# Performance work log

Hardware: AMD Instinct MI355X
Metric: run time of the kernel (lower is better)

The kernel has to match this reference:

```python
import jax, jax.numpy as jnp
import numpy as np

N_NODES = 100000
N_EDGES = 1600000


def setup_inputs() -> dict:
    key = jax.random.key(0)
    ks = jax.random.split(key, 12)
    s = lambda d: 1.0 / np.sqrt(d)
    inp = {
        "x": jax.random.normal(ks[0], (N_NODES, 64), dtype=jnp.float32),
        "edge_index": jax.random.randint(ks[1], (2, N_EDGES), 0, N_NODES, dtype=jnp.int64),
        "W_embed": jax.random.normal(ks[2], (64, 128), dtype=jnp.float32) * s(64),
        "eps1": jnp.zeros((), jnp.float32),
        "w1a": jax.random.normal(ks[3], (128, 128), dtype=jnp.float32) * s(128),
        "b1a": jnp.zeros((128,), jnp.float32),
        "w1b": jax.random.normal(ks[4], (128, 128), dtype=jnp.float32) * s(128),
        "b1b": jnp.zeros((128,), jnp.float32),
        "eps2": jnp.zeros((), jnp.float32),
        "w2a": jax.random.normal(ks[5], (128, 256), dtype=jnp.float32) * s(128),
        "b2a": jnp.zeros((256,), jnp.float32),
        "w2b": jax.random.normal(ks[6], (256, 128), dtype=jnp.float32) * s(256),
        "b2b": jnp.zeros((128,), jnp.float32),
        "eps3": jnp.zeros((), jnp.float32),
        "w3a": jax.random.normal(ks[7], (128, 256), dtype=jnp.float32) * s(128),
        "b3a": jnp.zeros((256,), jnp.float32),
        "w3b": jax.random.normal(ks[8], (256, 128), dtype=jnp.float32) * s(256),
        "b3b": jnp.zeros((128,), jnp.float32),
    }
    return inp


def _aggregate(h, src, dst, n):
    # GINConv sum aggregation: out[i] = sum_{(j,i) in E} h[j]
    return jax.ops.segment_sum(h[src], dst, num_segments=n)


def reference(x, edge_index, W_embed, eps1, w1a, b1a, w1b, b1b,
              eps2, w2a, b2a, w2b, b2b, eps3, w3a, b3a, w3b, b3b):
    src, dst = edge_index[0], edge_index[1]
    n = x.shape[0]
    # node_attr_encoder: linear embedding (dropout p=0 -> identity)
    h = x @ W_embed  # [N, dim]
    # conv1: nn((1+eps)*h + sum_neighbors), nn = Lin->ReLU->Lin
    z = (1.0 + eps1) * h + _aggregate(h, src, dst, n)
    h = jax.nn.relu(z @ w1a + b1a) @ w1b + b1b
    # conv2/conv3: nn = Lin->ReLU->Lin->ReLU
    z = (1.0 + eps2) * h + _aggregate(h, src, dst, n)
    h = jax.nn.relu(jax.nn.relu(z @ w2a + b2a) @ w2b + b2b)
    z = (1.0 + eps3) * h + _aggregate(h, src, dst, n)
    h = jax.nn.relu(jax.nn.relu(z @ w3a + b3a) @ w3b + b3b)
    return h
```

## Files before the change

kernel.cpp:

```cpp
#include <hip/hip_runtime.h>
#include <hip/hip_bf16.h>
#include <stdint.h>


typedef __attribute__((ext_vector_type(8))) short short8;
typedef __attribute__((ext_vector_type(16))) float float16v;

#define BKT 512
#define NBMAX 256

__device__ __forceinline__ float b2f_lo(unsigned int u) {
    return __uint_as_float(u << 16);
}
__device__ __forceinline__ float b2f_hi(unsigned int u) {
    return __uint_as_float(u & 0xffff0000u);
}
__device__ __forceinline__ unsigned short f2b(float f) {
    unsigned int u = __float_as_uint(f);
    return (unsigned short)((u + 0x7fffu + ((u >> 16) & 1u)) >> 16);
}

__global__ void detect_i64_kernel(const unsigned int* ei, int* flag) {
    if (threadIdx.x == 0) {
        int is64 = 1;
        for (int e = 0; e < 64; ++e)
            if (ei[2 * e + 1] != 0u) { is64 = 0; break; }
        *flag = is64;
    }
}

__device__ __forceinline__ int edge_at(const int* ei32, int is64, long long pos) {
    if (is64) return (int)(((const long long*)ei32)[pos]);
    return ei32[pos];
}

__global__ __launch_bounds__(256) void part_hist_kernel(
        const int* __restrict__ ei, const int* __restrict__ flag,
        int* __restrict__ bh, int E, int NB, int PB) {
    __shared__ int h[NBMAX];
    const int g = blockIdx.x, tid = threadIdx.x;
    const int is64 = *flag;
    for (int i = tid; i < NB; i += 256) h[i] = 0;
    __syncthreads();
    const int e0 = g * PB, e1 = min(e0 + PB, E);
    for (int e = e0 + tid; e < e1; e += 256) {
        int d = edge_at(ei, is64, (long long)E + e);
        atomicAdd(&h[d >> 9], 1);
    }
    __syncthreads();
    for (int i = tid; i < NB; i += 256) bh[i * gridDim.x + g] = h[i];
}

__global__ __launch_bounds__(1024) void scan1_kernel(
        const int* __restrict__ in, int* __restrict__ out,
        int* __restrict__ partial, int n) {
    __shared__ int sm[1024];
    const int t = threadIdx.x;
    const int i = blockIdx.x * 1024 + t;
    int v = (i < n) ? in[i] : 0;
    sm[t] = v;
    __syncthreads();
#pragma unroll
    for (int off = 1; off < 1024; off <<= 1) {
        int x = (t >= off) ? sm[t - off] : 0;
        __syncthreads();
        sm[t] += x;
        __syncthreads();
    }
    if (i < n) out[i] = sm[t] - v;
    if (t == 1023) partial[blockIdx.x] = sm[1023];
}

__global__ __launch_bounds__(256) void scan2_kernel(
        int* __restrict__ partial, int* __restrict__ blockoff, int g1) {
    __shared__ int sm[256];
    const int t = threadIdx.x;
    int v = (t < g1) ? partial[t] : 0;
    sm[t] = v;
    __syncthreads();
#pragma unroll
    for (int off = 1; off < 256; off <<= 1) {
        int x = (t >= off) ? sm[t - off] : 0;
        __syncthreads();
        sm[t] += x;
        __syncthreads();
    }
    blockoff[t] = sm[t] - v;
}

__global__ __launch_bounds__(1024) void scan3g_kernel(
        int* __restrict__ a, const int* __restrict__ blockoff, int n) {
    int i = blockIdx.x * 1024 + threadIdx.x;
    if (i < n) a[i] += blockoff[blockIdx.x];
}

__global__ __launch_bounds__(256) void part_scatter_kernel(
        const int* __restrict__ ei, const int* __restrict__ flag,
        const int* __restrict__ bhs, unsigned int* __restrict__ staged,
        int E, int NB, int PB) {
    __shared__ int cur[NBMAX];
    const int g = blockIdx.x, tid = threadIdx.x;
    const int is64 = *flag;
    for (int i = tid; i < NB; i += 256) cur[i] = bhs[i * gridDim.x + g];
    __syncthreads();
    const int e0 = g * PB, e1 = min(e0 + PB, E);
    for (int e = e0 + tid; e < e1; e += 256) {
        int d = edge_at(ei, is64, (long long)E + e);
        int s = edge_at(ei, is64, (long long)e);
        int b = d >> 9;
        int p = atomicAdd(&cur[b], 1);
        staged[p] = ((unsigned int)(d & (BKT - 1)) << 17) | (unsigned int)s;
    }
}

__global__ __launch_bounds__(256) void csr_local_kernel(
        const unsigned int* __restrict__ staged, const int* __restrict__ bhs,
        int* __restrict__ offs, int* __restrict__ csr, int N, int E, int NB, int G2) {
    __shared__ int hist[BKT];
    __shared__ int cur[BKT];
    const int b = blockIdx.x;
    const int tid = threadIdx.x;
    const int start = bhs[b * G2];
    const int end = (b + 1 < NB) ? bhs[(b + 1) * G2] : E;
    const int node0 = b * BKT;
    for (int i = tid; i < BKT; i += 256) hist[i] = 0;
    __syncthreads();
    for (int i = start + tid; i < end; i += 256)
        atomicAdd(&hist[staged[i] >> 17], 1);
    __syncthreads();
    const int i0 = tid * 2, i1 = i0 + 1;
    for (int off = 1; off < BKT; off <<= 1) {
        int v0 = (i0 >= off) ? hist[i0 - off] : 0;
        int v1 = (i1 >= off) ? hist[i1 - off] : 0;
        __syncthreads();
        hist[i0] += v0;
        hist[i1] += v1;
        __syncthreads();
    }
    for (int i = tid; i < BKT; i += 256) {
        int node = node0 + i;
        if (node < N) {
            int e0 = start + ((i == 0) ? 0 : hist[i - 1]);
            offs[node] = e0;
            cur[i] = e0;
        }
    }
    if (b == NB - 1 && tid == 0) offs[N] = E;
    __syncthreads();
    for (int i = start + tid; i < end; i += 256) {
        unsigned int v = staged[i];
        int dl = v >> 17;
        int src = (int)(v & 0x1ffff);
        int p = atomicAdd(&cur[dl], 1);
        csr[p] = src;
    }
}

__global__ void xconv_kernel(const float* __restrict__ x, unsigned short* __restrict__ xb,
                             int total_real, int total_pad) {
    int i = blockIdx.x * blockDim.x + threadIdx.x;
    if (i >= total_pad) return;
    xb[i] = (i < total_real) ? f2b(x[i]) : (unsigned short)0;
}

struct PW { const float* W; unsigned short* o; int K; int KOUT; };
struct PWAll { PW d[7]; int cum[8]; };

__global__ __launch_bounds__(256) void packall_kernel(PWAll P) {
    int id = blockIdx.x * blockDim.x + threadIdx.x;
    if (id >= P.cum[7]) return;
    int w = 0;
#pragma unroll
    for (int k = 1; k < 7; ++k) w += (id >= P.cum[k]);
    const int local = id - P.cum[w];
    const float* W = P.d[w].W;
    unsigned short* out = P.d[w].o;
    const int K = P.d[w].K, KOUT = P.d[w].KOUT;
    const int KS = K / 16;
    const int l = local & 63;
    const int s = (local >> 6) % KS;
    const int T = local / (KS * 64);
    const int kbase = s * 16 + ((l >> 5) << 3);
    const int n = T * 32 + (l & 31);
#pragma unroll
    for (int j = 0; j < 8; ++j)
        out[(long long)local * 8 + j] = f2b(W[(long long)(kbase + j) * KOUT + n]);
}

__global__ __launch_bounds__(256) void aggz_kernel(
        const unsigned short* __restrict__ H, const int* __restrict__ offs,
        const int* __restrict__ csr, const float* __restrict__ eps,
        unsigned short* __restrict__ Z, int n) {
    const int node = blockIdx.x * 16 + (threadIdx.x >> 4);
    const int c8 = (threadIdx.x & 15) << 3;
    if (node >= n) return;
    const int beg = offs[node];
    const int end = offs[node + 1];
    float a0 = 0.f, a1 = 0.f, a2 = 0.f, a3 = 0.f;
    float a4 = 0.f, a5 = 0.f, a6 = 0.f, a7 = 0.f;
    int i = beg;
    for (; i + 3 < end; i += 4) {
        const int j0 = csr[i], j1 = csr[i + 1], j2 = csr[i + 2], j3 = csr[i + 3];
        const uint4 u0 = *(const uint4*)(H + ((long long)j0 << 7) + c8);
        const uint4 u1 = *(const uint4*)(H + ((long long)j1 << 7) + c8);
        const uint4 u2 = *(const uint4*)(H + ((long long)j2 << 7) + c8);
        const uint4 u3 = *(const uint4*)(H + ((long long)j3 << 7) + c8);
        a0 += (b2f_lo(u0.x) + b2f_lo(u1.x)) + (b2f_lo(u2.x) + b2f_lo(u3.x));
        a1 += (b2f_hi(u0.x) + b2f_hi(u1.x)) + (b2f_hi(u2.x) + b2f_hi(u3.x));
        a2 += (b2f_lo(u0.y) + b2f_lo(u1.y)) + (b2f_lo(u2.y) + b2f_lo(u3.y));
        a3 += (b2f_hi(u0.y) + b2f_hi(u1.y)) + (b2f_hi(u2.y) + b2f_hi(u3.y));
        a4 += (b2f_lo(u0.z) + b2f_lo(u1.z)) + (b2f_lo(u2.z) + b2f_lo(u3.z));
        a5 += (b2f_hi(u0.z) + b2f_hi(u1.z)) + (b2f_hi(u2.z) + b2f_hi(u3.z));
        a6 += (b2f_lo(u0.w) + b2f_lo(u1.w)) + (b2f_lo(u2.w) + b2f_lo(u3.w));
        a7 += (b2f_hi(u0.w) + b2f_hi(u1.w)) + (b2f_hi(u2.w) + b2f_hi(u3.w));
    }
    for (; i < end; ++i) {
        const int j0 = csr[i];
        const uint4 u0 = *(const uint4*)(H + ((long long)j0 << 7) + c8);
        a0 += b2f_lo(u0.x); a1 += b2f_hi(u0.x);
        a2 += b2f_lo(u0.y); a3 += b2f_hi(u0.y);
        a4 += b2f_lo(u0.z); a5 += b2f_hi(u0.z);
        a6 += b2f_lo(u0.w); a7 += b2f_hi(u0.w);
    }
    const uint4 uh = *(const uint4*)(H + ((long long)node << 7) + c8);
    const float e = 1.0f + eps[0];
    a0 = fmaf(e, b2f_lo(uh.x), a0); a1 = fmaf(e, b2f_hi(uh.x), a1);
    a2 = fmaf(e, b2f_lo(uh.y), a2); a3 = fmaf(e, b2f_hi(uh.y), a3);
    a4 = fmaf(e, b2f_lo(uh.z), a4); a5 = fmaf(e, b2f_hi(uh.z), a5);
    a6 = fmaf(e, b2f_lo(uh.w), a6); a7 = fmaf(e, b2f_hi(uh.w), a7);
    uint4 o;
    o.x = ((unsigned int)f2b(a1) << 16) | (unsigned int)f2b(a0);
    o.y = ((unsigned int)f2b(a3) << 16) | (unsigned int)f2b(a2);
    o.z = ((unsigned int)f2b(a5) << 16) | (unsigned int)f2b(a4);
    o.w = ((unsigned int)f2b(a7) << 16) | (unsigned int)f2b(a6);
    *(uint4*)(Z + ((long long)node << 7) + c8) = o;
}

template<int KOUT, bool RELU, bool HASBIAS, bool OUTF32>
__device__ __forceinline__ void store_tile(float16v acc, long long row0, int col,
        const float* __restrict__ bias, void* __restrict__ outv, int Mreal) {
    const float bv = HASBIAS ? bias[col] : 0.f;
#pragma unroll
    for (int r = 0; r < 16; ++r) {
        float v = acc[r] + bv;
        if (RELU) v = fmaxf(v, 0.f);
        const long long row = row0 + (r & 3) + 8 * (r >> 2);
        if (OUTF32) {
            if (row < Mreal) ((float*)outv)[row * KOUT + col] = v;
        } else {
            ((unsigned short*)outv)[row * KOUT + col] = f2b(v);
        }
    }
}

template<int KIN, int KOUT, bool RELU, bool HASBIAS, bool OUTF32>
__global__ __launch_bounds__(256) void mm_mfma(
        const unsigned short* __restrict__ Zin, const unsigned short* __restrict__ Wp,
        const float* __restrict__ bias, void* __restrict__ outv, int Mreal) {
    constexpr int KS = KIN / 16;
    const int tid = threadIdx.x;
    const int w = tid >> 6;
    const int l = tid & 63;
    const int lm = l & 31;
    const int lk = l >> 5;
    const int wr = w & 1, wc = w >> 1;
    const long long R0 = (long long)blockIdx.x * 128 + wr * 64;
    const int C0 = blockIdx.y * 128 + wc * 64;
    const int T0 = C0 >> 5;

    const unsigned short* arow0 = Zin + (R0 + lm) * KIN + lk * 8;
    const unsigned short* arow1 = arow0 + 32 * KIN;
    const unsigned short* bb0 = Wp + ((long long)T0 * KS * 64 + l) * 8;
    const unsigned short* bb1 = Wp + ((long long)(T0 + 1) * KS * 64 + l) * 8;

    float16v acc00 = {}, acc01 = {}, acc10 = {}, acc11 = {};

#pragma unroll
    for (int s = 0; s < KS; ++s) {
        short8 a0 = *(const short8*)(arow0 + s * 16);
        short8 a1 = *(const short8*)(arow1 + s * 16);
        short8 b0 = *(const short8*)(bb0 + (long long)s * 64 * 8);
        short8 b1 = *(const short8*)(bb1 + (long long)s * 64 * 8);
        acc00 = __builtin_amdgcn_mfma_f32_32x32x16_bf16(a0, b0, acc00, 0, 0, 0);
        acc01 = __builtin_amdgcn_mfma_f32_32x32x16_bf16(a0, b1, acc01, 0, 0, 0);
        acc10 = __builtin_amdgcn_mfma_f32_32x32x16_bf16(a1, b0, acc10, 0, 0, 0);
        acc11 = __builtin_amdgcn_mfma_f32_32x32x16_bf16(a1, b1, acc11, 0, 0, 0);
    }

    const long long rbase = R0 + 4 * lk;
    store_tile<KOUT, RELU, HASBIAS, OUTF32>(acc00, rbase,      C0 + lm,      bias, outv, Mreal);
    store_tile<KOUT, RELU, HASBIAS, OUTF32>(acc01, rbase,      C0 + 32 + lm, bias, outv, Mreal);
    store_tile<KOUT, RELU, HASBIAS, OUTF32>(acc10, rbase + 32, C0 + lm,      bias, outv, Mreal);
    store_tile<KOUT, RELU, HASBIAS, OUTF32>(acc11, rbase + 32, C0 + 32 + lm, bias, outv, Mreal);
}

extern "C" void kernel_launch(void* const* d_in, const int* in_sizes, int n_in,
                              void* d_out, int out_size, void* d_ws, size_t ws_size,
                              hipStream_t stream) {
    const float* x    = (const float*)d_in[0];
    const int*   ei   = (const int*)d_in[1];
    const float* Wemb = (const float*)d_in[2];
    const float* eps1 = (const float*)d_in[3];
    const float* w1a  = (const float*)d_in[4];
    const float* b1a  = (const float*)d_in[5];
    const float* w1b  = (const float*)d_in[6];
    const float* b1b  = (const float*)d_in[7];
    const float* eps2 = (const float*)d_in[8];
    const float* w2a  = (const float*)d_in[9];
    const float* b2a  = (const float*)d_in[10];
    const float* w2b  = (const float*)d_in[11];
    const float* b2b  = (const float*)d_in[12];
    const float* eps3 = (const float*)d_in[13];
    const float* w3a  = (const float*)d_in[14];
    const float* b3a  = (const float*)d_in[15];
    const float* w3b  = (const float*)d_in[16];
    const float* b3b  = (const float*)d_in[17];

    const int N = in_sizes[0] / 64;
    const int E = in_sizes[1] / 2;
    const int Mpad = ((N + 127) / 128) * 128;
    const int NB = (N + BKT - 1) / BKT;
    const int G2 = 1024;
    const int PB = (E + G2 - 1) / G2;
    const int BH = NB * G2;

    char* ws = (char*)d_ws;
    size_t off = 0;
    auto alloc = [&](size_t bytes) -> void* {
        void* p = ws + off;
        off = (off + bytes + 255) & ~(size_t)255;
        return p;
    };
    unsigned short* xb  = (unsigned short*)alloc((size_t)Mpad * 64 * 2);
    unsigned short* Hb  = (unsigned short*)alloc((size_t)Mpad * 128 * 2);
    unsigned short* Zb  = (unsigned short*)alloc((size_t)Mpad * 128 * 2);
    unsigned short* Tb  = (unsigned short*)alloc((size_t)Mpad * 256 * 2);
    unsigned short* pWe = (unsigned short*)alloc((size_t)64 * 128 * 2);
    unsigned short* p1a = (unsigned short*)alloc((size_t)128 * 128 * 2);
    unsigned short* p1b = (unsigned short*)alloc((size_t)128 * 128 * 2);
    unsigned short* p2a = (unsigned short*)alloc((size_t)128 * 256 * 2);
    unsigned short* p2b = (unsigned short*)alloc((size_t)256 * 128 * 2);
    unsigned short* p3a = (unsigned short*)alloc((size_t)128 * 256 * 2);
    unsigned short* p3b = (unsigned short*)alloc((size_t)256 * 128 * 2);
    int* offs = (int*)alloc((size_t)(N + 1) * 4);
    int* csr  = (int*)alloc((size_t)E * 4);
    int* bh   = (int*)alloc((size_t)BH * 4);
    int* bhs  = (int*)alloc((size_t)BH * 4);
    int* part = (int*)alloc(1024);
    int* boff = (int*)alloc(1024);
    int* flag = (int*)alloc(256);

    unsigned int* staged = (unsigned int*)Tb;

    detect_i64_kernel<<<1, 64, 0, stream>>>((const unsigned int*)ei, flag);
    part_hist_kernel<<<G2, 256, 0, stream>>>(ei, flag, bh, E, NB, PB);
    const int G1 = (BH + 1023) / 1024;
    scan1_kernel<<<G1, 1024, 0, stream>>>(bh, bhs, part, BH);
    scan2_kernel<<<1, 256, 0, stream>>>(part, boff, G1);
    scan3g_kernel<<<G1, 1024, 0, stream>>>(bhs, boff, BH);
    part_scatter_kernel<<<G2, 256, 0, stream>>>(ei, flag, bhs, staged, E, NB, PB);
    csr_local_kernel<<<NB, 256, 0, stream>>>(staged, bhs, offs, csr, N, E, NB, G2);

    xconv_kernel<<<(Mpad * 64 + 255) / 256, 256, 0, stream>>>(x, xb, N * 64, Mpad * 64);
    {
        PWAll P;
        const PW descs[7] = {
            {Wemb, pWe, 64, 128}, {w1a, p1a, 128, 128}, {w1b, p1b, 128, 128},
            {w2a, p2a, 128, 256}, {w2b, p2b, 256, 128}, {w3a, p3a, 128, 256},
            {w3b, p3b, 256, 128}};
        int c = 0;
        for (int k = 0; k < 7; ++k) {
            P.d[k] = descs[k];
            P.cum[k] = c;
            c += (descs[k].KOUT / 32) * (descs[k].K / 16) * 64;
        }
        P.cum[7] = c;
        packall_kernel<<<(c + 255) / 256, 256, 0, stream>>>(P);
    }

    const int MMB = Mpad / 128;
    const int AGB = (N + 15) / 16;
    const dim3 g1(MMB, 1), g2(MMB, 2);

    mm_mfma<64, 128, false, false, false><<<g1, 256, 0, stream>>>(xb, pWe, nullptr, Hb, N);

    aggz_kernel<<<AGB, 256, 0, stream>>>(Hb, offs, csr, eps1, Zb, N);
    mm_mfma<128, 128, true,  true, false><<<g1, 256, 0, stream>>>(Zb, p1a, b1a, Tb, N);
    mm_mfma<128, 128, false, true, false><<<g1, 256, 0, stream>>>(Tb, p1b, b1b, Hb, N);

    aggz_kernel<<<AGB, 256, 0, stream>>>(Hb, offs, csr, eps2, Zb, N);
    mm_mfma<128, 256, true, true, false><<<g2, 256, 0, stream>>>(Zb, p2a, b2a, Tb, N);
    mm_mfma<256, 128, true, true, false><<<g1, 256, 0, stream>>>(Tb, p2b, b2b, Hb, N);

    aggz_kernel<<<AGB, 256, 0, stream>>>(Hb, offs, csr, eps3, Zb, N);
    mm_mfma<128, 256, true, true, false><<<g2, 256, 0, stream>>>(Zb, p3a, b3a, Tb, N);
    mm_mfma<256, 128, true, true, true><<<g1, 256, 0, stream>>>(Tb, p3b, b3b, d_out, N);
}
```

Baseline: 510.2 us.

## Fuse neighbor aggregation with both MLP GEMMs per GIN layer in one kernel

Each GIN layer now runs as one kernel. Every 128-row block gathers and sums neighbor features into swizzled LDS, runs the first GEMM with bias and ReLU into LDS, then accumulates the second GEMM, so the Z and hidden T intermediates no longer go through global memory. The embedding GEMM now reads the fp32 input directly and converts it to bf16 in registers, which removes the separate conversion kernel and its buffer. In exchange, each block uses 64KB of LDS, which limits how many blocks fit per CU. The latency-bound gather phase now runs at lower occupancy and with fewer threads per node batch than the standalone aggregation kernel.

```diff
diff --git a/kernel.cpp b/kernel.cpp
--- a/kernel.cpp
+++ b/kernel.cpp
@@ -156,13 +156,6 @@
     }
 }
 
-__global__ void xconv_kernel(const float* __restrict__ x, unsigned short* __restrict__ xb,
-                             int total_real, int total_pad) {
-    int i = blockIdx.x * blockDim.x + threadIdx.x;
-    if (i >= total_pad) return;
-    xb[i] = (i < total_real) ? f2b(x[i]) : (unsigned short)0;
-}
-
 struct PW { const float* W; unsigned short* o; int K; int KOUT; };
 struct PWAll { PW d[7]; int cum[8]; };
 
@@ -187,77 +180,10 @@
         out[(long long)local * 8 + j] = f2b(W[(long long)(kbase + j) * KOUT + n]);
 }
 
-__global__ __launch_bounds__(256) void aggz_kernel(
-        const unsigned short* __restrict__ H, const int* __restrict__ offs,
-        const int* __restrict__ csr, const float* __restrict__ eps,
-        unsigned short* __restrict__ Z, int n) {
-    const int node = blockIdx.x * 16 + (threadIdx.x >> 4);
-    const int c8 = (threadIdx.x & 15) << 3;
-    if (node >= n) return;
-    const int beg = offs[node];
-    const int end = offs[node + 1];
-    float a0 = 0.f, a1 = 0.f, a2 = 0.f, a3 = 0.f;
-    float a4 = 0.f, a5 = 0.f, a6 = 0.f, a7 = 0.f;
-    int i = beg;
-    for (; i + 3 < end; i += 4) {
-        const int j0 = csr[i], j1 = csr[i + 1], j2 = csr[i + 2], j3 = csr[i + 3];
-        const uint4 u0 = *(const uint4*)(H + ((long long)j0 << 7) + c8);
-        const uint4 u1 = *(const uint4*)(H + ((long long)j1 << 7) + c8);
-        const uint4 u2 = *(const uint4*)(H + ((long long)j2 << 7) + c8);
-        const uint4 u3 = *(const uint4*)(H + ((long long)j3 << 7) + c8);
-        a0 += (b2f_lo(u0.x) + b2f_lo(u1.x)) + (b2f_lo(u2.x) + b2f_lo(u3.x));
-        a1 += (b2f_hi(u0.x) + b2f_hi(u1.x)) + (b2f_hi(u2.x) + b2f_hi(u3.x));
-        a2 += (b2f_lo(u0.y) + b2f_lo(u1.y)) + (b2f_lo(u2.y) + b2f_lo(u3.y));
-        a3 += (b2f_hi(u0.y) + b2f_hi(u1.y)) + (b2f_hi(u2.y) + b2f_hi(u3.y));
-        a4 += (b2f_lo(u0.z) + b2f_lo(u1.z)) + (b2f_lo(u2.z) + b2f_lo(u3.z));
-        a5 += (b2f_hi(u0.z) + b2f_hi(u1.z)) + (b2f_hi(u2.z) + b2f_hi(u3.z));
-        a6 += (b2f_lo(u0.w) + b2f_lo(u1.w)) + (b2f_lo(u2.w) + b2f_lo(u3.w));
-        a7 += (b2f_hi(u0.w) + b2f_hi(u1.w)) + (b2f_hi(u2.w) + b2f_hi(u3.w));
-    }
-    for (; i < end; ++i) {
-        const int j0 = csr[i];
-        const uint4 u0 = *(const uint4*)(H + ((long long)j0 << 7) + c8);
-        a0 += b2f_lo(u0.x); a1 += b2f_hi(u0.x);
-        a2 += b2f_lo(u0.y); a3 += b2f_hi(u0.y);
-        a4 += b2f_lo(u0.z); a5 += b2f_hi(u0.z);
-        a6 += b2f_lo(u0.w); a7 += b2f_hi(u0.w);
-    }
-    const uint4 uh = *(const uint4*)(H + ((long long)node << 7) + c8);
-    const float e = 1.0f + eps[0];
-    a0 = fmaf(e, b2f_lo(uh.x), a0); a1 = fmaf(e, b2f_hi(uh.x), a1);
-    a2 = fmaf(e, b2f_lo(uh.y), a2); a3 = fmaf(e, b2f_hi(uh.y), a3);
-    a4 = fmaf(e, b2f_lo(uh.z), a4); a5 = fmaf(e, b2f_hi(uh.z), a5);
-    a6 = fmaf(e, b2f_lo(uh.w), a6); a7 = fmaf(e, b2f_hi(uh.w), a7);
-    uint4 o;
-    o.x = ((unsigned int)f2b(a1) << 16) | (unsigned int)f2b(a0);
-    o.y = ((unsigned int)f2b(a3) << 16) | (unsigned int)f2b(a2);
-    o.z = ((unsigned int)f2b(a5) << 16) | (unsigned int)f2b(a4);
-    o.w = ((unsigned int)f2b(a7) << 16) | (unsigned int)f2b(a6);
-    *(uint4*)(Z + ((long long)node << 7) + c8) = o;
-}
-
-template<int KOUT, bool RELU, bool HASBIAS, bool OUTF32>
-__device__ __forceinline__ void store_tile(float16v acc, long long row0, int col,
-        const float* __restrict__ bias, void* __restrict__ outv, int Mreal) {
-    const float bv = HASBIAS ? bias[col] : 0.f;
-#pragma unroll
-    for (int r = 0; r < 16; ++r) {
-        float v = acc[r] + bv;
-        if (RELU) v = fmaxf(v, 0.f);
-        const long long row = row0 + (r & 3) + 8 * (r >> 2);
-        if (OUTF32) {
-            if (row < Mreal) ((float*)outv)[row * KOUT + col] = v;
-        } else {
-            ((unsigned short*)outv)[row * KOUT + col] = f2b(v);
-        }
-    }
-}
-
-template<int KIN, int KOUT, bool RELU, bool HASBIAS, bool OUTF32>
-__global__ __launch_bounds__(256) void mm_mfma(
-        const unsigned short* __restrict__ Zin, const unsigned short* __restrict__ Wp,
-        const float* __restrict__ bias, void* __restrict__ outv, int Mreal) {
-    constexpr int KS = KIN / 16;
+__global__ __launch_bounds__(256) void mm_embed(
+        const float* __restrict__ X, const unsigned short* __restrict__ Wp,
+        unsigned short* __restrict__ out, int Mreal) {
+    constexpr int KS = 4;
     const int tid = threadIdx.x;
     const int w = tid >> 6;
     const int l = tid & 63;
@@ -265,20 +191,31 @@
     const int lk = l >> 5;
     const int wr = w & 1, wc = w >> 1;
     const long long R0 = (long long)blockIdx.x * 128 + wr * 64;
-    const int C0 = blockIdx.y * 128 + wc * 64;
-    const int T0 = C0 >> 5;
-
-    const unsigned short* arow0 = Zin + (R0 + lm) * KIN + lk * 8;
-    const unsigned short* arow1 = arow0 + 32 * KIN;
+    const int T0 = (wc * 64) >> 5;
+
+    const long long r0 = (R0 + lm < Mreal) ? (R0 + lm) : (Mreal - 1);
+    const long long r1 = (R0 + 32 + lm < Mreal) ? (R0 + 32 + lm) : (Mreal - 1);
+    const float* xr0 = X + r0 * 64 + lk * 8;
+    const float* xr1 = X + r1 * 64 + lk * 8;
     const unsigned short* bb0 = Wp + ((long long)T0 * KS * 64 + l) * 8;
     const unsigned short* bb1 = Wp + ((long long)(T0 + 1) * KS * 64 + l) * 8;
 
     float16v acc00 = {}, acc01 = {}, acc10 = {}, acc11 = {};
-
 #pragma unroll
     for (int s = 0; s < KS; ++s) {
-        short8 a0 = *(const short8*)(arow0 + s * 16);
-        short8 a1 = *(const short8*)(arow1 + s * 16);
+        float4 f0a = *(const float4*)(xr0 + s * 16);
+        float4 f0b = *(const float4*)(xr0 + s * 16 + 4);
+        float4 f1a = *(const float4*)(xr1 + s * 16);
+        float4 f1b = *(const float4*)(xr1 + s * 16 + 4);
+        short8 a0, a1;
+        a0[0] = (short)f2b(f0a.x); a0[1] = (short)f2b(f0a.y);
+        a0[2] = (short)f2b(f0a.z); a0[3] = (short)f2b(f0a.w);
+        a0[4] = (short)f2b(f0b.x); a0[5] = (short)f2b(f0b.y);
+        a0[6] = (short)f2b(f0b.z); a0[7] = (short)f2b(f0b.w);
+        a1[0] = (short)f2b(f1a.x); a1[1] = (short)f2b(f1a.y);
+        a1[2] = (short)f2b(f1a.z); a1[3] = (short)f2b(f1a.w);
+        a1[4] = (short)f2b(f1b.x); a1[5] = (short)f2b(f1b.y);
+        a1[6] = (short)f2b(f1b.z); a1[7] = (short)f2b(f1b.w);
         short8 b0 = *(const short8*)(bb0 + (long long)s * 64 * 8);
         short8 b1 = *(const short8*)(bb1 + (long long)s * 64 * 8);
         acc00 = __builtin_amdgcn_mfma_f32_32x32x16_bf16(a0, b0, acc00, 0, 0, 0);
@@ -286,12 +223,170 @@
         acc10 = __builtin_amdgcn_mfma_f32_32x32x16_bf16(a1, b0, acc10, 0, 0, 0);
         acc11 = __builtin_amdgcn_mfma_f32_32x32x16_bf16(a1, b1, acc11, 0, 0, 0);
     }
-
+    auto st = [&](float16v acc, long long rb, int col) {
+#pragma unroll
+        for (int r = 0; r < 16; ++r) {
+            long long row = rb + (r & 3) + 8 * (r >> 2);
+            out[row * 128 + col] = f2b(acc[r]);
+        }
+    };
     const long long rbase = R0 + 4 * lk;
-    store_tile<KOUT, RELU, HASBIAS, OUTF32>(acc00, rbase,      C0 + lm,      bias, outv, Mreal);
-    store_tile<KOUT, RELU, HASBIAS, OUTF32>(acc01, rbase,      C0 + 32 + lm, bias, outv, Mreal);
-    store_tile<KOUT, RELU, HASBIAS, OUTF32>(acc10, rbase + 32, C0 + lm,      bias, outv, Mreal);
-    store_tile<KOUT, RELU, HASBIAS, OUTF32>(acc11, rbase + 32, C0 + 32 + lm, bias, outv, Mreal);
+    st(acc00, rbase,      wc * 64 + lm);
+    st(acc01, rbase,      wc * 64 + 32 + lm);
+    st(acc10, rbase + 32, wc * 64 + lm);
+    st(acc11, rbase + 32, wc * 64 + 32 + lm);
+}
+
+template<int KMID, bool RELU2, bool OUTF32>
+__global__ __launch_bounds__(256) void fused_layer(
+        const unsigned short* __restrict__ Hin, const int* __restrict__ offs,
+        const int* __restrict__ csr, const float* __restrict__ eps,
+        const unsigned short* __restrict__ Wap, const float* __restrict__ ba,
+        const unsigned short* __restrict__ Wbp, const float* __restrict__ bb,
+        void* __restrict__ outp, int Mreal) {
+    __shared__ unsigned short lds[32768];
+    const int tid = threadIdx.x;
+    const int R0 = blockIdx.x * 128;
+    const float e1 = 1.0f + eps[0];
+
+    {
+        const int c8 = (tid & 15) << 3;
+        const int sec = c8 >> 3;
+#pragma unroll 1
+        for (int p = 0; p < 8; ++p) {
+            const int row = p * 16 + (tid >> 4);
+            const int node = R0 + row;
+            float a0 = 0.f, a1 = 0.f, a2 = 0.f, a3 = 0.f;
+            float a4 = 0.f, a5 = 0.f, a6 = 0.f, a7 = 0.f;
+            if (node < Mreal) {
+                const int beg = offs[node];
+                const int end = offs[node + 1];
+                int i = beg;
+                for (; i + 3 < end; i += 4) {
+                    const int j0 = csr[i], j1 = csr[i + 1], j2 = csr[i + 2], j3 = csr[i + 3];
+                    const uint4 u0 = *(const uint4*)(Hin + ((long long)j0 << 7) + c8);
+                    const uint4 u1 = *(const uint4*)(Hin + ((long long)j1 << 7) + c8);
+                    const uint4 u2 = *(const uint4*)(Hin + ((long long)j2 << 7) + c8);
+                    const uint4 u3 = *(const uint4*)(Hin + ((long long)j3 << 7) + c8);
+                    a0 += (b2f_lo(u0.x) + b2f_lo(u1.x)) + (b2f_lo(u2.x) + b2f_lo(u3.x));
+                    a1 += (b2f_hi(u0.x) + b2f_hi(u1.x)) + (b2f_hi(u2.x) + b2f_hi(u3.x));
+                    a2 += (b2f_lo(u0.y) + b2f_lo(u1.y)) + (b2f_lo(u2.y) + b2f_lo(u3.y));
+                    a3 += (b2f_hi(u0.y) + b2f_hi(u1.y)) + (b2f_hi(u2.y) + b2f_hi(u3.y));
+                    a4 += (b2f_lo(u0.z) + b2f_lo(u1.z)) + (b2f_lo(u2.z) + b2f_lo(u3.z));
+                    a5 += (b2f_hi(u0.z) + b2f_hi(u1.z)) + (b2f_hi(u2.z) + b2f_hi(u3.z));
+                    a6 += (b2f_lo(u0.w) + b2f_lo(u1.w)) + (b2f_lo(u2.w) + b2f_lo(u3.w));
+                    a7 += (b2f_hi(u0.w) + b2f_hi(u1.w)) + (b2f_hi(u2.w) + b2f_hi(u3.w));
+                }
+                for (; i < end; ++i) {
+                    const uint4 u0 = *(const uint4*)(Hin + ((long long)csr[i] << 7) + c8);
+                    a0 += b2f_lo(u0.x); a1 += b2f_hi(u0.x);
+                    a2 += b2f_lo(u0.y); a3 += b2f_hi(u0.y);
+                    a4 += b2f_lo(u0.z); a5 += b2f_hi(u0.z);
+                    a6 += b2f_lo(u0.w); a7 += b2f_hi(u0.w);
+                }
+                const uint4 uh = *(const uint4*)(Hin + ((long long)node << 7) + c8);
+                a0 = fmaf(e1, b2f_lo(uh.x), a0); a1 = fmaf(e1, b2f_hi(uh.x), a1);
+                a2 = fmaf(e1, b2f_lo(uh.y), a2); a3 = fmaf(e1, b2f_hi(uh.y), a3);
+                a4 = fmaf(e1, b2f_lo(uh.z), a4); a5 = fmaf(e1, b2f_hi(uh.z), a5);
+                a6 = fmaf(e1, b2f_lo(uh.w), a6); a7 = fmaf(e1, b2f_hi(uh.w), a7);
+            }
+            uint4 o;
+            o.x = ((unsigned int)f2b(a1) << 16) | (unsigned int)f2b(a0);
+            o.y = ((unsigned int)f2b(a3) << 16) | (unsigned int)f2b(a2);
+            o.z = ((unsigned int)f2b(a5) << 16) | (unsigned int)f2b(a4);
+            o.w = ((unsigned int)f2b(a7) << 16) | (unsigned int)f2b(a6);
+            const int slot = sec * 128 + (row ^ (sec & 7));
+            *(uint4*)&lds[slot * 8] = o;
+        }
+    }
+    __syncthreads();
+
+    const int w = tid >> 6;
+    const int l = tid & 63;
+    const int lm = l & 31;
+    const int lk = l >> 5;
+    const int wr = w & 1, wc = w >> 1;
+    constexpr int KS1 = 8;
+    constexpr int KSB = KMID / 16;
+    constexpr int NH = KMID / 128;
+
+    float16v d00 = {}, d01 = {}, d10 = {}, d11 = {};
+
+    for (int h = 0; h < NH; ++h) {
+        if (h) __syncthreads();
+
+        {
+            float16v c00 = {}, c01 = {}, c10 = {}, c11 = {};
+            const int T1 = (wc * 64 + h * 128) >> 5;
+            const unsigned short* bp0 = Wap + ((long long)T1 * KS1 * 64 + l) * 8;
+            const unsigned short* bp1 = Wap + ((long long)(T1 + 1) * KS1 * 64 + l) * 8;
+#pragma unroll
+            for (int s = 0; s < KS1; ++s) {
+                const int sec = s * 2 + lk;
+                short8 a0 = *(const short8*)&lds[(sec * 128 + ((wr * 64 + lm) ^ (sec & 7))) * 8];
+                short8 a1 = *(const short8*)&lds[(sec * 128 + ((wr * 64 + 32 + lm) ^ (sec & 7))) * 8];
+                short8 b0 = *(const short8*)(bp0 + (long long)s * 64 * 8);
+                short8 b1 = *(const short8*)(bp1 + (long long)s * 64 * 8);
+                c00 = __builtin_amdgcn_mfma_f32_32x32x16_bf16(a0, b0, c00, 0, 0, 0);
+                c01 = __builtin_amdgcn_mfma_f32_32x32x16_bf16(a0, b1, c01, 0, 0, 0);
+                c10 = __builtin_amdgcn_mfma_f32_32x32x16_bf16(a1, b0, c10, 0, 0, 0);
+                c11 = __builtin_amdgcn_mfma_f32_32x32x16_bf16(a1, b1, c11, 0, 0, 0);
+            }
+            auto wT = [&](float16v acc, int rbase, int cl) {
+                const float bv = ba[h * 128 + cl];
+                const int secT = cl >> 3;
+                const int cj = cl & 7;
+#pragma unroll
+                for (int r = 0; r < 16; ++r) {
+                    float v = fmaxf(acc[r] + bv, 0.f);
+                    const int row = rbase + (r & 3) + 8 * (r >> 2);
+                    lds[(2048 + secT * 128 + (row ^ (secT & 7))) * 8 + cj] = f2b(v);
+                }
+            };
+            wT(c00, wr * 64 + 4 * lk,      wc * 64 + lm);
+            wT(c01, wr * 64 + 4 * lk,      wc * 64 + 32 + lm);
+            wT(c10, wr * 64 + 32 + 4 * lk, wc * 64 + lm);
+            wT(c11, wr * 64 + 32 + 4 * lk, wc * 64 + 32 + lm);
+        }
+        __syncthreads();
+
+        {
+            const int T2 = (wc * 64) >> 5;
+            const unsigned short* bp0 = Wbp + ((long long)T2 * KSB * 64 + l) * 8;
+            const unsigned short* bp1 = Wbp + ((long long)(T2 + 1) * KSB * 64 + l) * 8;
+#pragma unroll
+            for (int s = 0; s < 8; ++s) {
+                const int sec = s * 2 + lk;
+                short8 a0 = *(const short8*)&lds[(2048 + sec * 128 + ((wr * 64 + lm) ^ (sec & 7))) * 8];
+                short8 a1 = *(const short8*)&lds[(2048 + sec * 128 + ((wr * 64 + 32 + lm) ^ (sec & 7))) * 8];
+                short8 b0 = *(const short8*)(bp0 + (long long)(h * 8 + s) * 64 * 8);
+                short8 b1 = *(const short8*)(bp1 + (long long)(h * 8 + s) * 64 * 8);
+                d00 = __builtin_amdgcn_mfma_f32_32x32x16_bf16(a0, b0, d00, 0, 0, 0);
+                d01 = __builtin_amdgcn_mfma_f32_32x32x16_bf16(a0, b1, d01, 0, 0, 0);
+                d10 = __builtin_amdgcn_mfma_f32_32x32x16_bf16(a1, b0, d10, 0, 0, 0);
+                d11 = __builtin_amdgcn_mfma_f32_32x32x16_bf16(a1, b1, d11, 0, 0, 0);
+            }
+        }
+    }
+
+    auto st = [&](float16v acc, int rbase, int col) {
+        const float bv = bb[col];
+#pragma unroll
+        for (int r = 0; r < 16; ++r) {
+            float v = acc[r] + bv;
+            if (RELU2) v = fmaxf(v, 0.f);
+            const long long row = (long long)R0 + rbase + (r & 3) + 8 * (r >> 2);
+            if (OUTF32) {
+                if (row < Mreal) ((float*)outp)[row * 128 + col] = v;
+            } else {
+                ((unsigned short*)outp)[row * 128 + col] = f2b(v);
+            }
+        }
+    };
+    st(d00, wr * 64 + 4 * lk,      wc * 64 + lm);
+    st(d01, wr * 64 + 4 * lk,      wc * 64 + 32 + lm);
+    st(d10, wr * 64 + 32 + 4 * lk, wc * 64 + lm);
+    st(d11, wr * 64 + 32 + 4 * lk, wc * 64 + 32 + lm);
 }
 
 extern "C" void kernel_launch(void* const* d_in, const int* in_sizes, int n_in,
@@ -331,10 +426,8 @@
         off = (off + bytes + 255) & ~(size_t)255;
         return p;
     };
-    unsigned short* xb  = (unsigned short*)alloc((size_t)Mpad * 64 * 2);
-    unsigned short* Hb  = (unsigned short*)alloc((size_t)Mpad * 128 * 2);
-    unsigned short* Zb  = (unsigned short*)alloc((size_t)Mpad * 128 * 2);
-    unsigned short* Tb  = (unsigned short*)alloc((size_t)Mpad * 256 * 2);
+    unsigned short* Ha  = (unsigned short*)alloc((size_t)Mpad * 128 * 2);
+    unsigned short* Hb2 = (unsigned short*)alloc((size_t)Mpad * 128 * 2);
     unsigned short* pWe = (unsigned short*)alloc((size_t)64 * 128 * 2);
     unsigned short* p1a = (unsigned short*)alloc((size_t)128 * 128 * 2);
     unsigned short* p1b = (unsigned short*)alloc((size_t)128 * 128 * 2);
@@ -344,13 +437,12 @@
     unsigned short* p3b = (unsigned short*)alloc((size_t)256 * 128 * 2);
     int* offs = (int*)alloc((size_t)(N + 1) * 4);
     int* csr  = (int*)alloc((size_t)E * 4);
+    unsigned int* staged = (unsigned int*)alloc((size_t)E * 4);
     int* bh   = (int*)alloc((size_t)BH * 4);
     int* bhs  = (int*)alloc((size_t)BH * 4);
     int* part = (int*)alloc(1024);
     int* boff = (int*)alloc(1024);
     int* flag = (int*)alloc(256);
-
-    unsigned int* staged = (unsigned int*)Tb;
 
     detect_i64_kernel<<<1, 64, 0, stream>>>((const unsigned int*)ei, flag);
     part_hist_kernel<<<G2, 256, 0, stream>>>(ei, flag, bh, E, NB, PB);
@@ -361,7 +453,6 @@
     part_scatter_kernel<<<G2, 256, 0, stream>>>(ei, flag, bhs, staged, E, NB, PB);
     csr_local_kernel<<<NB, 256, 0, stream>>>(staged, bhs, offs, csr, N, E, NB, G2);
 
-    xconv_kernel<<<(Mpad * 64 + 255) / 256, 256, 0, stream>>>(x, xb, N * 64, Mpad * 64);
     {
         PWAll P;
         const PW descs[7] = {
@@ -379,20 +470,15 @@
     }
 
     const int MMB = Mpad / 128;
-    const int AGB = (N + 15) / 16;
-    const dim3 g1(MMB, 1), g2(MMB, 2);
-
-    mm_mfma<64, 128, false, false, false><<<g1, 256, 0, stream>>>(xb, pWe, nullptr, Hb, N);
-
-    aggz_kernel<<<AGB, 256, 0, stream>>>(Hb, offs, csr, eps1, Zb, N);
-    mm_mfma<128, 128, true,  true, false><<<g1, 256, 0, stream>>>(Zb, p1a, b1a, Tb, N);
-    mm_mfma<128, 128, false, true, false><<<g1, 256, 0, stream>>>(Tb, p1b, b1b, Hb, N);
-
-    aggz_kernel<<<AGB, 256, 0, stream>>>(Hb, offs, csr, eps2, Zb, N);
-    mm_mfma<128, 256, true, true, false><<<g2, 256, 0, stream>>>(Zb, p2a, b2a, Tb, N);
-    mm_mfma<256, 128, true, true, false><<<g1, 256, 0, stream>>>(Tb, p2b, b2b, Hb, N);
-
-    aggz_kernel<<<AGB, 256, 0, stream>>>(Hb, offs, csr, eps3, Zb, N);
-    mm_mfma<128, 256, true, true, false><<<g2, 256, 0, stream>>>(Zb, p3a, b3a, Tb, N);
-    mm_mfma<256, 128, true, true, true><<<g1, 256, 0, stream>>>(Tb, p3b, b3b, d_out, N);
-}
+
+    mm_embed<<<MMB, 256, 0, stream>>>(x, pWe, Ha, N);
+
+    fused_layer<128, false, false><<<MMB, 256, 0, stream>>>(
+        Ha, offs, csr, eps1, p1a, b1a, p1b, b1b, Hb2, N);
+
+    fused_layer<256, true, false><<<MMB, 256, 0, stream>>>(
+        Hb2, offs, csr, eps2, p2a, b2a, p2b, b2b, Ha, N);
+
+    fused_layer<256, true, true><<<MMB, 256, 0, stream>>>(
+        Ha, offs, csr, eps3, p3a, b3a, p3b, b3b, d_out, N);
+}
```

New measurement: 839.4 us. +64.5%, slower.
